# Kernel optimization log

Measured on AMD Instinct MI355X. Metric: run time of the kernel, lower is better.

The kernel has to match this reference:

```python
import jax, jax.numpy as jnp
import numpy as np

B, G, FI, FO, H, W = 16, 8, 64, 64, 64, 64
N_ITER = 3


def setup_inputs() -> dict:
    key = jax.random.key(0)
    kx, kw, kb = jax.random.split(key, 3)
    x = jax.random.normal(kx, (B, G * FI, H, W), dtype=jnp.float32)
    # kaiming_normal_ on [fo*g, fi, 1, 1]: std = sqrt(2 / fan_in), fan_in = fi*1*1
    weight = jax.random.normal(kw, (FO * G, FI, 1, 1), dtype=jnp.float32) * np.sqrt(2.0 / FI)
    bias = jax.random.normal(kb, (1, FO, 1, 1), dtype=jnp.float32) * 0.01
    return {"x": x, "weight": weight, "bias": bias}


def reference(x, weight, bias):
    g, n_iter = G, N_ITER
    gfo, fi = weight.shape[:2]
    fo = gfo // g
    b, c, h, w = x.shape
    # grouped 1x1 conv == per-group channel matmul
    xg = x.reshape(b, g, fi, h, w)
    wg = weight.reshape(g, fo, fi)
    con = jnp.einsum('bgihw,gfi->bgfhw', xg, wg)  # [B, g, fo, H, W]
    beta = jnp.zeros((), dtype=x.dtype)
    for i in range(n_iter):
        alpha = jax.nn.sigmoid(beta)
        v = jnp.sum(alpha * con, axis=1, keepdims=True)  # [B, 1, fo, H, W]
        if i == n_iter - 1:
            out = v[:, 0]  # [B, fo, H, W]
            return out + bias
        beta = beta + jnp.sum(v * con, axis=2, keepdims=True)  # [B, g, 1, H, W]
```

## Files before the change

### kernel.cpp

```cpp
#include <hip/hip_runtime.h>


typedef __attribute__((ext_vector_type(8))) _Float16 half8;
typedef __attribute__((ext_vector_type(4))) float f32x4;

#define NG   8
#define NFI  64
#define NFO  64
#define HW   4096
#define PT   64
#define XPAD 72

__device__ __forceinline__ float sigmoidf_fast(float v) {
    float e = __builtin_amdgcn_exp2f(-1.44269504088896f * v);
    return __builtin_amdgcn_rcpf(1.0f + e);
}

__global__ __launch_bounds__(256)
void wconv_kernel(const float* __restrict__ w, _Float16* __restrict__ wh,
                  _Float16* __restrict__ wl) {
    int idx = (blockIdx.x * 256 + threadIdx.x) * 4;
    f32x4 v = *(const f32x4*)(w + idx);
    _Float16 h[4], l[4];
    #pragma unroll
    for (int k = 0; k < 4; ++k) {
        h[k] = (_Float16)v[k];
        l[k] = (_Float16)(v[k] - (float)h[k]);
    }
    *(ulong1*)(wh + idx) = *(ulong1*)h;
    *(ulong1*)(wl + idx) = *(ulong1*)l;
}

__global__ __launch_bounds__(256, 2)
void routing_kernel(const float* __restrict__ x,
                    const _Float16* __restrict__ wh,
                    const _Float16* __restrict__ wl,
                    const float* __restrict__ bias,
                    float* __restrict__ out) {
    __shared__ __align__(16) _Float16 xs[NG * PT * XPAD];

    const int tid = threadIdx.x;
    const int b   = blockIdx.x >> 6;
    const int p0  = (blockIdx.x & 63) << 6;

    const float* xb = x + (size_t)b * (NG * NFI) * HW + p0;

    #pragma unroll 8
    for (int j = 0; j < 32; ++j) {
        int flat = j * 256 + tid;
        int row  = flat >> 4;
        int pc   = (flat & 15) << 2;
        f32x4 v = *(const f32x4*)(xb + (size_t)row * HW + pc);
        int g = row >> 6, i = row & 63;
        _Float16* basep = xs + (g * PT) * XPAD + i;
        basep[(pc + 0) * XPAD] = (_Float16)v[0];
        basep[(pc + 1) * XPAD] = (_Float16)v[1];
        basep[(pc + 2) * XPAD] = (_Float16)v[2];
        basep[(pc + 3) * XPAD] = (_Float16)v[3];
    }
    __syncthreads();

    const int lane = tid & 63;
    const int wv   = tid >> 6;
    const int pl   = lane & 15;
    const int q    = lane >> 4;
    const int pw   = wv * 16 + pl;

    f32x4 acc[NG][4];
    #pragma unroll
    for (int g = 0; g < NG; ++g)
        #pragma unroll
        for (int t = 0; t < 4; ++t)
            acc[g][t] = (f32x4){0.f, 0.f, 0.f, 0.f};

    #pragma unroll
    for (int g = 0; g < NG; ++g) {
        const _Float16* xrow = xs + (g * PT + pw) * XPAD;
        half8 b0 = *(const half8*)(xrow + q * 8);
        half8 b1 = *(const half8*)(xrow + 32 + q * 8);
        const int wgoff = g * (NFO * NFI);
        #pragma unroll
        for (int t = 0; t < 4; ++t) {
            const int roff = wgoff + (t * 16 + pl) * NFI + q * 8;
            half8 a0h = *(const half8*)(wh + roff);
            half8 a1h = *(const half8*)(wh + roff + 32);
            half8 a0l = *(const half8*)(wl + roff);
            half8 a1l = *(const half8*)(wl + roff + 32);
            acc[g][t] = __builtin_amdgcn_mfma_f32_16x16x32_f16(a0h, b0, acc[g][t], 0, 0, 0);
            acc[g][t] = __builtin_amdgcn_mfma_f32_16x16x32_f16(a1h, b1, acc[g][t], 0, 0, 0);
            acc[g][t] = __builtin_amdgcn_mfma_f32_16x16x32_f16(a0l, b0, acc[g][t], 0, 0, 0);
            acc[g][t] = __builtin_amdgcn_mfma_f32_16x16x32_f16(a1l, b1, acc[g][t], 0, 0, 0);
        }
    }

    float v0[4][4];
    #pragma unroll
    for (int t = 0; t < 4; ++t)
        #pragma unroll
        for (int r = 0; r < 4; ++r) {
            float s = 0.f;
            #pragma unroll
            for (int g = 0; g < NG; ++g) s += acc[g][t][r];
            v0[t][r] = 0.5f * s;
        }

    float beta[NG], alpha[NG];
    #pragma unroll
    for (int g = 0; g < NG; ++g) {
        float s = 0.f;
        #pragma unroll
        for (int t = 0; t < 4; ++t)
            #pragma unroll
            for (int r = 0; r < 4; ++r)
                s += v0[t][r] * acc[g][t][r];
        s += __shfl_xor(s, 16);
        s += __shfl_xor(s, 32);
        beta[g]  = s;
        alpha[g] = sigmoidf_fast(s);
    }

    #pragma unroll
    for (int t = 0; t < 4; ++t)
        #pragma unroll
        for (int r = 0; r < 4; ++r) {
            float s = 0.f;
            #pragma unroll
            for (int g = 0; g < NG; ++g) s += alpha[g] * acc[g][t][r];
            v0[t][r] = s;
        }
    #pragma unroll
    for (int g = 0; g < NG; ++g) {
        float s = 0.f;
        #pragma unroll
        for (int t = 0; t < 4; ++t)
            #pragma unroll
            for (int r = 0; r < 4; ++r)
                s += v0[t][r] * acc[g][t][r];
        s += __shfl_xor(s, 16);
        s += __shfl_xor(s, 32);
        beta[g] += s;
        alpha[g] = sigmoidf_fast(beta[g]);
    }

    #pragma unroll
    for (int t = 0; t < 4; ++t)
        #pragma unroll
        for (int r = 0; r < 4; ++r) {
            int f = t * 16 + q * 4 + r;
            float s = bias[f];
            #pragma unroll
            for (int g = 0; g < NG; ++g) s += alpha[g] * acc[g][t][r];
            out[((size_t)(b * NFO + f)) * HW + p0 + pw] = s;
        }
}

extern "C" void kernel_launch(void* const* d_in, const int* in_sizes, int n_in,
                              void* d_out, int out_size, void* d_ws, size_t ws_size,
                              hipStream_t stream) {
    const float* x    = (const float*)d_in[0];
    const float* w    = (const float*)d_in[1];
    const float* bias = (const float*)d_in[2];
    float* out = (float*)d_out;
    _Float16* wh = (_Float16*)d_ws;
    _Float16* wl = wh + NG * NFO * NFI;

    wconv_kernel<<<32, 256, 0, stream>>>(w, wh, wl);
    routing_kernel<<<1024, 256, 0, stream>>>(x, wh, wl, bias, out);
}
```

Measured before the change: 247.3 us.

## Load x directly into registers and prepack weights in MFMA fragment order

Drops the LDS staging of the x tile: each lane reads its fp32 x values straight from global memory into registers, one group ahead in a double buffer, and converts them to fp16 for the MFMA B operand. The weight conversion kernel now writes hi/lo fp16 weights already in per-lane fragment order, so every weight load is one contiguous 16-byte read per lane. This removes the shared-memory transposed stores and the block barrier. The cost is that global x loads become per-lane strided scalar reads (16 loads per group, each row 4096 floats apart) with poorer coalescing, plus higher register pressure from the prefetch buffers.

```diff
diff --git a/kernel.cpp b/kernel.cpp
--- a/kernel.cpp
+++ b/kernel.cpp
@@ -8,8 +8,6 @@
 #define NFI  64
 #define NFO  64
 #define HW   4096
-#define PT   64
-#define XPAD 72
 
 __device__ __forceinline__ float sigmoidf_fast(float v) {
     float e = __builtin_amdgcn_exp2f(-1.44269504088896f * v);
@@ -17,54 +15,39 @@
 }
 
 __global__ __launch_bounds__(256)
-void wconv_kernel(const float* __restrict__ w, _Float16* __restrict__ wh,
-                  _Float16* __restrict__ wl) {
-    int idx = (blockIdx.x * 256 + threadIdx.x) * 4;
-    f32x4 v = *(const f32x4*)(w + idx);
-    _Float16 h[4], l[4];
+void wconv_kernel(const float* __restrict__ w, _Float16* __restrict__ wbuf) {
+    int V = blockIdx.x * 256 + threadIdx.x;
+    int g    = V >> 10;
+    int t    = (V >> 8) & 3;
+    int c    = (V >> 6) & 3;
+    int lane = V & 63;
+    int pl = lane & 15, q = lane >> 4;
+    const float* src = w + g * (NFO * NFI) + (t * 16 + pl) * NFI + (c & 1) * 32 + q * 8;
+    half8 o;
     #pragma unroll
-    for (int k = 0; k < 4; ++k) {
-        h[k] = (_Float16)v[k];
-        l[k] = (_Float16)(v[k] - (float)h[k]);
+    for (int j = 0; j < 8; ++j) {
+        float f = src[j];
+        _Float16 h = (_Float16)f;
+        o[j] = (c >> 1) ? (_Float16)(f - (float)h) : h;
     }
-    *(ulong1*)(wh + idx) = *(ulong1*)h;
-    *(ulong1*)(wl + idx) = *(ulong1*)l;
+    *(half8*)(wbuf + (size_t)V * 8) = o;
 }
 
 __global__ __launch_bounds__(256, 2)
 void routing_kernel(const float* __restrict__ x,
-                    const _Float16* __restrict__ wh,
-                    const _Float16* __restrict__ wl,
+                    const _Float16* __restrict__ wbuf,
                     const float* __restrict__ bias,
                     float* __restrict__ out) {
-    __shared__ __align__(16) _Float16 xs[NG * PT * XPAD];
-
-    const int tid = threadIdx.x;
-    const int b   = blockIdx.x >> 6;
-    const int p0  = (blockIdx.x & 63) << 6;
-
-    const float* xb = x + (size_t)b * (NG * NFI) * HW + p0;
-
-    #pragma unroll 8
-    for (int j = 0; j < 32; ++j) {
-        int flat = j * 256 + tid;
-        int row  = flat >> 4;
-        int pc   = (flat & 15) << 2;
-        f32x4 v = *(const f32x4*)(xb + (size_t)row * HW + pc);
-        int g = row >> 6, i = row & 63;
-        _Float16* basep = xs + (g * PT) * XPAD + i;
-        basep[(pc + 0) * XPAD] = (_Float16)v[0];
-        basep[(pc + 1) * XPAD] = (_Float16)v[1];
-        basep[(pc + 2) * XPAD] = (_Float16)v[2];
-        basep[(pc + 3) * XPAD] = (_Float16)v[3];
-    }
-    __syncthreads();
-
+    const int tid  = threadIdx.x;
+    const int b    = blockIdx.x >> 6;
+    const int p0   = (blockIdx.x & 63) << 6;
     const int lane = tid & 63;
     const int wv   = tid >> 6;
     const int pl   = lane & 15;
     const int q    = lane >> 4;
     const int pw   = wv * 16 + pl;
+
+    const float* xg = x + (size_t)b * (NG * NFI) * HW + p0 + pw;
 
     f32x4 acc[NG][4];
     #pragma unroll
@@ -73,25 +56,47 @@
         for (int t = 0; t < 4; ++t)
             acc[g][t] = (f32x4){0.f, 0.f, 0.f, 0.f};
 
+    float xv0[16], xv1[16];
+    #define LOADX(G, V)                                                  \
+        {                                                                \
+            const float* p_ = xg + (size_t)((G) * 64 + q * 8) * HW;      \
+            _Pragma("unroll")                                            \
+            for (int j = 0; j < 8; ++j) {                                \
+                (V)[j]     = p_[(size_t)j * HW];                         \
+                (V)[8 + j] = p_[(size_t)(32 + j) * HW];                  \
+            }                                                            \
+        }
+
+    LOADX(0, xv0);
+
     #pragma unroll
     for (int g = 0; g < NG; ++g) {
-        const _Float16* xrow = xs + (g * PT + pw) * XPAD;
-        half8 b0 = *(const half8*)(xrow + q * 8);
-        half8 b1 = *(const half8*)(xrow + 32 + q * 8);
-        const int wgoff = g * (NFO * NFI);
+        float* cur = (g & 1) ? xv1 : xv0;
+        float* nxt = (g & 1) ? xv0 : xv1;
+        if (g < NG - 1) LOADX(g + 1, nxt);
+
+        half8 b0, b1;
+        #pragma unroll
+        for (int j = 0; j < 8; ++j) {
+            b0[j] = (_Float16)cur[j];
+            b1[j] = (_Float16)cur[8 + j];
+        }
+
+        const _Float16* wg = wbuf + ((size_t)g * 4) * 4 * 512 + lane * 8;
         #pragma unroll
         for (int t = 0; t < 4; ++t) {
-            const int roff = wgoff + (t * 16 + pl) * NFI + q * 8;
-            half8 a0h = *(const half8*)(wh + roff);
-            half8 a1h = *(const half8*)(wh + roff + 32);
-            half8 a0l = *(const half8*)(wl + roff);
-            half8 a1l = *(const half8*)(wl + roff + 32);
+            const _Float16* wp = wg + (size_t)t * 4 * 512;
+            half8 a0h = *(const half8*)(wp);
+            half8 a1h = *(const half8*)(wp + 512);
+            half8 a0l = *(const half8*)(wp + 1024);
+            half8 a1l = *(const half8*)(wp + 1536);
             acc[g][t] = __builtin_amdgcn_mfma_f32_16x16x32_f16(a0h, b0, acc[g][t], 0, 0, 0);
             acc[g][t] = __builtin_amdgcn_mfma_f32_16x16x32_f16(a1h, b1, acc[g][t], 0, 0, 0);
             acc[g][t] = __builtin_amdgcn_mfma_f32_16x16x32_f16(a0l, b0, acc[g][t], 0, 0, 0);
             acc[g][t] = __builtin_amdgcn_mfma_f32_16x16x32_f16(a1l, b1, acc[g][t], 0, 0, 0);
         }
     }
+    #undef LOADX
 
     float v0[4][4];
     #pragma unroll
@@ -161,9 +166,8 @@
     const float* w    = (const float*)d_in[1];
     const float* bias = (const float*)d_in[2];
     float* out = (float*)d_out;
-    _Float16* wh = (_Float16*)d_ws;
-    _Float16* wl = wh + NG * NFO * NFI;
+    _Float16* wbuf = (_Float16*)d_ws;
 
-    wconv_kernel<<<32, 256, 0, stream>>>(w, wh, wl);
-    routing_kernel<<<1024, 256, 0, stream>>>(x, wh, wl, bias, out);
+    wconv_kernel<<<32, 256, 0, stream>>>(w, wbuf);
+    routing_kernel<<<1024, 256, 0, stream>>>(x, wbuf, bias, out);
 }
```

After: 215.5 us. 1.15x faster.
